# Kernel optimization log

Measured on AMD Instinct MI355X. Metric: run time of the kernel, lower is better.

The kernel has to match this reference:

```python
import jax, jax.numpy as jnp
import numpy as np

N_NODES, N_FEAT, EIG, HID = 20000, 128, 32, 64
N_EDGES = 640000
TEMP = 1.0
NUM_DROP = int(N_NODES * N_FEAT * 0.1)  # num_drop_ratio = 0.1
EPS_LOG = 1e-8


def setup_inputs() -> dict:
    key = jax.random.key(0)
    ks = jax.random.split(key, 9)
    x = jax.random.normal(ks[0], (N_NODES, N_FEAT), dtype=jnp.float32)
    edge_index = jax.random.randint(ks[1], (2, N_EDGES), 0, N_NODES, dtype=jnp.int64)
    edge_weights = jax.random.uniform(ks[2], (N_EDGES,), dtype=jnp.float32)
    x_eigen_distance = jax.random.normal(ks[3], (N_NODES, N_FEAT, EIG), dtype=jnp.float32)
    uni_rand = jax.random.uniform(ks[4], (N_NODES * N_FEAT, 2), dtype=jnp.float32,
                                  minval=1e-6, maxval=1.0 - 1e-6)
    # prob_encoder params: Linear(EIG->HID), ReLU, Linear(HID->2)
    W1 = jax.random.normal(ks[5], (EIG, HID), dtype=jnp.float32) / np.sqrt(EIG)
    b1 = jnp.zeros((HID,), dtype=jnp.float32)
    W2 = jax.random.normal(ks[6], (HID, 2), dtype=jnp.float32) / np.sqrt(HID)
    b2 = jnp.zeros((2,), dtype=jnp.float32)
    return {"x": x, "edge_index": edge_index, "edge_weights": edge_weights,
            "x_eigen_distance": x_eigen_distance, "uni_rand": uni_rand,
            "W1": W1, "b1": b1, "W2": W2, "b2": b2}


def reference(x, edge_index, edge_weights, x_eigen_distance, uni_rand, W1, b1, W2, b2):
    # flatten to [N_NODES*N_FEAT, EIG]
    flat = x_eigen_distance.reshape(-1, x_eigen_distance.shape[-1])
    h = jax.nn.relu(flat @ W1 + b1)          # [M, HID]
    logits = h @ W2 + b2                     # [M, 2]
    logits = jnp.log(jax.nn.softmax(logits, axis=1) + EPS_LOG)
    gumbel = -jnp.log(-jnp.log(uni_rand))    # gumbel noise from uniform
    y = jax.nn.softmax((logits + gumbel) / TEMP, axis=1)
    poss = jnp.clip(1.0 - y[:, 0], 1e-6, 1.0)  # [M]
    neg_vals, idx = jax.lax.top_k(-poss, NUM_DROP)  # smallest NUM_DROP
    vals = -neg_vals
    x_new = x.reshape(-1).at[idx].multiply(vals).reshape(x.shape)
    return x_new, edge_index, edge_weights
```

## Files before the change

kernel.cpp:

```cpp
#include <hip/hip_runtime.h>
#include <hip/hip_bf16.h>

#define N_NODES 20000
#define N_FEAT  128
#define EIG     32
#define HID     64
#define N_EDGES 640000
#define M_ROWS  (N_NODES * N_FEAT)
#define K_DROP  256000
#define NBINS   16384
#define LIST_CAP 4096
#define NTILES  (M_ROWS / 16)
#define NBLK    2560

#define POSS_BYTES ((size_t)M_ROWS * 4)
#define HIST_BYTES (NBINS * 4)
#define META_WORDS 16

typedef __attribute__((ext_vector_type(8))) short short8;
typedef __attribute__((ext_vector_type(4))) float floatx4;

__device__ __forceinline__ short f2bf(float f) {
  unsigned u = __float_as_uint(f);
  unsigned r = u + 0x7fffu + ((u >> 16) & 1u);
  return (short)(r >> 16);
}

__device__ __forceinline__ short2 f2bf2(float x, float y) {
  float2 f; f.x = x; f.y = y;
  __hip_bfloat162 h = __float22bfloat162_rn(f);
  union { __hip_bfloat162 h2; short2 s2; } u;
  u.h2 = h;
  return u.s2;
}

__device__ __forceinline__ int bin_of(float ps) {
  int b = (int)(ps * (float)NBINS);
  if (b > NBINS - 1) b = NBINS - 1;
  if (b < 0) b = 0;
  return b;
}

__global__ __launch_bounds__(256) void poss_kernel(
    const float* __restrict__ eig, const float* __restrict__ uni,
    const float* __restrict__ W1, const float* __restrict__ b1,
    const float* __restrict__ W2, const float* __restrict__ b2,
    float* __restrict__ poss, unsigned* __restrict__ hist)
{
  const int wave = threadIdx.x >> 6;
  const int lane = threadIdx.x & 63;
  const int col  = lane & 15;
  const int quad = lane >> 4;

  short8 bfrag[4];
  #pragma unroll
  for (int t = 0; t < 4; ++t)
    #pragma unroll
    for (int j = 0; j < 8; ++j)
      bfrag[t][j] = f2bf(W1[(quad * 8 + j) * HID + 16 * t + col]);

  float b1v[4], wd[4];
  #pragma unroll
  for (int t = 0; t < 4; ++t) {
    int n = 16 * t + col;
    b1v[t] = b1[n];
    wd[t] = W2[2 * n + 1] - W2[2 * n + 0];
  }
  const float bd = b2[1] - b2[0];

  for (int tile = blockIdx.x * 4 + wave; tile < NTILES; tile += NBLK * 4) {
    const int rowbase = tile * 16;

    const float4* pa = (const float4*)(eig + (size_t)(rowbase + col) * EIG + quad * 8);
    float4 v0 = pa[0], v1 = pa[1];
    union { short8 v; short2 h[4]; } au;
    au.h[0] = f2bf2(v0.x, v0.y);
    au.h[1] = f2bf2(v0.z, v0.w);
    au.h[2] = f2bf2(v1.x, v1.y);
    au.h[3] = f2bf2(v1.z, v1.w);

    floatx4 c[4];
    const floatx4 z = {0.f, 0.f, 0.f, 0.f};
    #pragma unroll
    for (int t = 0; t < 4; ++t)
      c[t] = __builtin_amdgcn_mfma_f32_16x16x32_bf16(au.v, bfrag[t], z, 0, 0, 0);

    float pd[4] = {0, 0, 0, 0};
    #pragma unroll
    for (int t = 0; t < 4; ++t)
      #pragma unroll
      for (int r = 0; r < 4; ++r) {
        float h = fmaxf(c[t][r] + b1v[t], 0.0f);
        pd[r] = fmaf(h, wd[t], pd[r]);
      }

    #pragma unroll
    for (int s = 1; s < 16; s <<= 1)
      #pragma unroll
      for (int r = 0; r < 4; ++r)
        pd[r] += __shfl_xor(pd[r], s, 64);

    if (col < 4) {
      int r = col;
      float ldiff = ((r == 0) ? pd[0] : (r == 1) ? pd[1] : (r == 2) ? pd[2] : pd[3]) + bd;
      int row = rowbase + quad * 4 + r;

      const float2 u = *(const float2*)(uni + (size_t)row * 2);
      float t = __expf(ldiff);
      float e1t = 1e-8f * (1.0f + t);
      float A = t + e1t;
      float B = 1.0f + e1t;
      float Lx = -__logf(u.x);
      float Ly = -__logf(u.y);
      float num = A * Lx;
      float ps = __fdividef(num, num + B * Ly);
      ps = fminf(fmaxf(ps, 1e-6f), 1.0f);
      poss[row] = ps;
      atomicAdd(&hist[bin_of(ps)], 1u);
    }
  }
}

__global__ void scan_kernel(const unsigned* __restrict__ hist, unsigned* __restrict__ meta)
{
  __shared__ unsigned psum[256];
  int t = threadIdx.x;
  unsigned s = 0;
  for (int i = 0; i < NBINS / 256; ++i) s += hist[t * (NBINS / 256) + i];
  psum[t] = s;
  __syncthreads();
  if (t == 0) {
    unsigned cum = 0;
    int c = 0;
    for (; c < 256; ++c) {
      if (cum + psum[c] >= K_DROP) break;
      cum += psum[c];
    }
    int b = c * (NBINS / 256);
    for (;; ++b) {
      unsigned h = hist[b];
      if (cum + h >= K_DROP) break;
      cum += h;
    }
    meta[0] = (unsigned)b;
    meta[1] = cum;
  }
}

__global__ __launch_bounds__(256) void collect_kernel(
    const float* __restrict__ poss, unsigned* __restrict__ meta,
    unsigned* __restrict__ list)
{
  int i = blockIdx.x * 256 + threadIdx.x;
  if (i >= M_ROWS) return;
  float ps = poss[i];
  if (bin_of(ps) == (int)meta[0]) {
    unsigned p = atomicAdd(&meta[7], 1u);
    if (p < LIST_CAP) list[p] = (unsigned)i;
  }
}

__global__ void rank_kernel(const float* __restrict__ poss,
                            const unsigned* __restrict__ list,
                            unsigned* __restrict__ meta)
{
  __shared__ unsigned sk[LIST_CAP];
  __shared__ unsigned si[LIST_CAP];
  unsigned n = meta[7];
  if (n > LIST_CAP) n = LIST_CAP;
  unsigned target = K_DROP - meta[1] - 1;
  int t = threadIdx.x;
  for (unsigned i = t; i < n; i += 256) {
    unsigned ix = list[i];
    si[i] = ix;
    sk[i] = __float_as_uint(poss[ix]);
  }
  __syncthreads();
  for (unsigned el = t; el < n; el += 256) {
    unsigned k = sk[el], ix = si[el];
    unsigned r = 0;
    for (unsigned j = 0; j < n; ++j)
      r += (sk[j] < k) || (sk[j] == k && si[j] < ix);
    if (r == target) { meta[2] = k; meta[3] = ix; }
  }
}

__global__ __launch_bounds__(256) void finalize_kernel(
    const float* __restrict__ x, const float* __restrict__ poss,
    const int* __restrict__ ei, const float* __restrict__ ew,
    const unsigned* __restrict__ meta, float* __restrict__ out)
{
  unsigned i = blockIdx.x * 256 + threadIdx.x;
  if (i < M_ROWS) {
    unsigned T = meta[2], cut = meta[3];
    float ps = poss[i];
    unsigned k = __float_as_uint(ps);
    bool sel = (k < T) || (k == T && i <= cut);
    float xv = x[i];
    out[i] = sel ? xv * ps : xv;
  } else if (i < M_ROWS + 2 * N_EDGES) {
    unsigned j = i - M_ROWS;
    out[i] = (float)ei[j];
  } else if (i < M_ROWS + 2 * N_EDGES + N_EDGES) {
    unsigned j = i - (M_ROWS + 2 * N_EDGES);
    out[i] = ew[j];
  }
}

extern "C" void kernel_launch(void* const* d_in, const int* in_sizes, int n_in,
                              void* d_out, int out_size, void* d_ws, size_t ws_size,
                              hipStream_t stream)
{
  const float* x   = (const float*)d_in[0];
  const int*   ei  = (const int*)d_in[1];
  const float* ew  = (const float*)d_in[2];
  const float* eig = (const float*)d_in[3];
  const float* uni = (const float*)d_in[4];
  const float* W1  = (const float*)d_in[5];
  const float* b1  = (const float*)d_in[6];
  const float* W2  = (const float*)d_in[7];
  const float* b2  = (const float*)d_in[8];
  float* out = (float*)d_out;

  char* ws = (char*)d_ws;
  float*    poss = (float*)ws;
  unsigned* hist = (unsigned*)(ws + POSS_BYTES);
  unsigned* meta = (unsigned*)(ws + POSS_BYTES + HIST_BYTES);
  unsigned* list = (unsigned*)(ws + POSS_BYTES + HIST_BYTES + META_WORDS * 4);

  hipMemsetAsync(hist, 0, HIST_BYTES + META_WORDS * 4 + LIST_CAP * 4, stream);
  poss_kernel<<<NBLK, 256, 0, stream>>>(eig, uni, W1, b1, W2, b2, poss, hist);
  scan_kernel<<<1, 256, 0, stream>>>(hist, meta);
  collect_kernel<<<M_ROWS / 256, 256, 0, stream>>>(poss, meta, list);
  rank_kernel<<<1, 256, 0, stream>>>(poss, list, meta);
  finalize_kernel<<<(M_ROWS + 2 * N_EDGES + N_EDGES) / 256, 256, 0, stream>>>(
      x, poss, ei, ew, meta, out);
}
```

Before: 539.1 us.

## Prefetch next tile in poss kernel, parallel scan, vectorize collect/finalize, move edge copy

The poss kernel now software-pipelines its loads, fetching the next tile's eigen rows and uniform noise while computing the current one. The single-thread histogram walk in the scan kernel is replaced by a shared-memory parallel prefix sum plus a short serial walk within one chunk. The collect and finalize kernels are vectorized to float4. The edge index/weight copy moves from finalize into collect, making finalize smaller. The prefetch raises register pressure, and these are several independent changes.

New measurement: 532.0 us. About the same (-1.3%).

```diff
diff --git a/kernel.cpp b/kernel.cpp
--- a/kernel.cpp
+++ b/kernel.cpp
@@ -51,6 +51,7 @@
   const int lane = threadIdx.x & 63;
   const int col  = lane & 15;
   const int quad = lane >> 4;
+  const int STR  = NBLK * 4;
 
   short8 bfrag[4];
   #pragma unroll
@@ -68,11 +69,29 @@
   }
   const float bd = b2[1] - b2[0];
 
-  for (int tile = blockIdx.x * 4 + wave; tile < NTILES; tile += NBLK * 4) {
+  const bool epi = (col < 4);
+  const int  epirow = quad * 4 + col;
+
+  int tile = blockIdx.x * 4 + wave;
+  float4 v0 = {0,0,0,0}, v1 = {0,0,0,0};
+  float2 u0 = {0.5f, 0.5f};
+  if (tile < NTILES) {
+    const float4* pa = (const float4*)(eig + (size_t)(tile * 16 + col) * EIG + quad * 8);
+    v0 = pa[0]; v1 = pa[1];
+    if (epi) u0 = *(const float2*)(uni + (size_t)(tile * 16 + epirow) * 2);
+  }
+
+  for (; tile < NTILES; tile += STR) {
+    const int nxt = tile + STR;
+    float4 n0 = {0,0,0,0}, n1 = {0,0,0,0};
+    float2 nu = {0.5f, 0.5f};
+    if (nxt < NTILES) {
+      const float4* pn = (const float4*)(eig + (size_t)(nxt * 16 + col) * EIG + quad * 8);
+      n0 = pn[0]; n1 = pn[1];
+      if (epi) nu = *(const float2*)(uni + (size_t)(nxt * 16 + epirow) * 2);
+    }
+
     const int rowbase = tile * 16;
-
-    const float4* pa = (const float4*)(eig + (size_t)(rowbase + col) * EIG + quad * 8);
-    float4 v0 = pa[0], v1 = pa[1];
     union { short8 v; short2 h[4]; } au;
     au.h[0] = f2bf2(v0.x, v0.y);
     au.h[1] = f2bf2(v0.z, v0.w);
@@ -100,63 +119,91 @@
       for (int r = 0; r < 4; ++r)
         pd[r] += __shfl_xor(pd[r], s, 64);
 
-    if (col < 4) {
+    if (epi) {
       int r = col;
       float ldiff = ((r == 0) ? pd[0] : (r == 1) ? pd[1] : (r == 2) ? pd[2] : pd[3]) + bd;
-      int row = rowbase + quad * 4 + r;
-
-      const float2 u = *(const float2*)(uni + (size_t)row * 2);
+      int row = rowbase + epirow;
+
       float t = __expf(ldiff);
       float e1t = 1e-8f * (1.0f + t);
       float A = t + e1t;
       float B = 1.0f + e1t;
-      float Lx = -__logf(u.x);
-      float Ly = -__logf(u.y);
+      float Lx = -__logf(u0.x);
+      float Ly = -__logf(u0.y);
       float num = A * Lx;
       float ps = __fdividef(num, num + B * Ly);
       ps = fminf(fmaxf(ps, 1e-6f), 1.0f);
       poss[row] = ps;
       atomicAdd(&hist[bin_of(ps)], 1u);
     }
+
+    v0 = n0; v1 = n1; u0 = nu;
   }
 }
 
 __global__ void scan_kernel(const unsigned* __restrict__ hist, unsigned* __restrict__ meta)
 {
   __shared__ unsigned psum[256];
+  __shared__ unsigned chunkbins[64];
+  __shared__ unsigned selc, selcum;
   int t = threadIdx.x;
   unsigned s = 0;
+  #pragma unroll 4
   for (int i = 0; i < NBINS / 256; ++i) s += hist[t * (NBINS / 256) + i];
   psum[t] = s;
   __syncthreads();
+  for (int off = 1; off < 256; off <<= 1) {
+    unsigned add = (t >= off) ? psum[t - off] : 0u;
+    __syncthreads();
+    psum[t] += add;
+    __syncthreads();
+  }
+  unsigned incl = psum[t];
+  unsigned excl = incl - s;
+  if (excl < K_DROP && K_DROP <= incl) { selc = (unsigned)t; selcum = excl; }
+  __syncthreads();
+  unsigned c = selc;
+  if (t < NBINS / 256) chunkbins[t] = hist[c * (NBINS / 256) + t];
+  __syncthreads();
   if (t == 0) {
-    unsigned cum = 0;
-    int c = 0;
-    for (; c < 256; ++c) {
-      if (cum + psum[c] >= K_DROP) break;
-      cum += psum[c];
-    }
-    int b = c * (NBINS / 256);
-    for (;; ++b) {
-      unsigned h = hist[b];
-      if (cum + h >= K_DROP) break;
+    unsigned cum = selcum;
+    int b = (int)c * (NBINS / 256);
+    for (int i = 0; i < NBINS / 256; ++i) {
+      unsigned h = chunkbins[i];
+      if (cum + h >= K_DROP) { meta[0] = (unsigned)(b + i); meta[1] = cum; break; }
       cum += h;
     }
-    meta[0] = (unsigned)b;
-    meta[1] = cum;
   }
 }
 
 __global__ __launch_bounds__(256) void collect_kernel(
     const float* __restrict__ poss, unsigned* __restrict__ meta,
-    unsigned* __restrict__ list)
+    unsigned* __restrict__ list,
+    const int* __restrict__ ei, const float* __restrict__ ew,
+    float* __restrict__ out)
 {
   int i = blockIdx.x * 256 + threadIdx.x;
-  if (i >= M_ROWS) return;
-  float ps = poss[i];
-  if (bin_of(ps) == (int)meta[0]) {
-    unsigned p = atomicAdd(&meta[7], 1u);
-    if (p < LIST_CAP) list[p] = (unsigned)i;
+  if (i < M_ROWS / 4) {
+    float4 p = ((const float4*)poss)[i];
+    int B = (int)meta[0];
+    float pp[4] = {p.x, p.y, p.z, p.w};
+    #pragma unroll
+    for (int j = 0; j < 4; ++j) {
+      if (bin_of(pp[j]) == B) {
+        unsigned q = atomicAdd(&meta[7], 1u);
+        if (q < LIST_CAP) list[q] = (unsigned)(4 * i + j);
+      }
+    }
+  } else {
+    int j = (i - M_ROWS / 4) * 4;
+    if (j < 2 * N_EDGES) {
+      int4 e = *(const int4*)(ei + j);
+      *(float4*)(out + M_ROWS + j) =
+          make_float4((float)e.x, (float)e.y, (float)e.z, (float)e.w);
+    } else {
+      int k = j - 2 * N_EDGES;
+      *(float4*)(out + M_ROWS + j) = *(const float4*)(ew + k);
+    }
   }
 }
 
@@ -187,24 +234,24 @@
 
 __global__ __launch_bounds__(256) void finalize_kernel(
     const float* __restrict__ x, const float* __restrict__ poss,
-    const int* __restrict__ ei, const float* __restrict__ ew,
     const unsigned* __restrict__ meta, float* __restrict__ out)
 {
-  unsigned i = blockIdx.x * 256 + threadIdx.x;
-  if (i < M_ROWS) {
-    unsigned T = meta[2], cut = meta[3];
-    float ps = poss[i];
-    unsigned k = __float_as_uint(ps);
-    bool sel = (k < T) || (k == T && i <= cut);
-    float xv = x[i];
-    out[i] = sel ? xv * ps : xv;
-  } else if (i < M_ROWS + 2 * N_EDGES) {
-    unsigned j = i - M_ROWS;
-    out[i] = (float)ei[j];
-  } else if (i < M_ROWS + 2 * N_EDGES + N_EDGES) {
-    unsigned j = i - (M_ROWS + 2 * N_EDGES);
-    out[i] = ew[j];
-  }
+  int i = blockIdx.x * 256 + threadIdx.x;
+  if (i >= M_ROWS / 4) return;
+  unsigned T = meta[2], cut = meta[3];
+  float4 xv = ((const float4*)x)[i];
+  float4 pv = ((const float4*)poss)[i];
+  float xx[4] = {xv.x, xv.y, xv.z, xv.w};
+  float pp[4] = {pv.x, pv.y, pv.z, pv.w};
+  float o[4];
+  #pragma unroll
+  for (int j = 0; j < 4; ++j) {
+    unsigned k = __float_as_uint(pp[j]);
+    unsigned idx = (unsigned)(4 * i + j);
+    bool sel = (k < T) || (k == T && idx <= cut);
+    o[j] = sel ? xx[j] * pp[j] : xx[j];
+  }
+  ((float4*)out)[i] = make_float4(o[0], o[1], o[2], o[3]);
 }
 
 extern "C" void kernel_launch(void* const* d_in, const int* in_sizes, int n_in,
@@ -231,8 +278,7 @@
   hipMemsetAsync(hist, 0, HIST_BYTES + META_WORDS * 4 + LIST_CAP * 4, stream);
   poss_kernel<<<NBLK, 256, 0, stream>>>(eig, uni, W1, b1, W2, b2, poss, hist);
   scan_kernel<<<1, 256, 0, stream>>>(hist, meta);
-  collect_kernel<<<M_ROWS / 256, 256, 0, stream>>>(poss, meta, list);
+  collect_kernel<<<2500 + 1875, 256, 0, stream>>>(poss, meta, list, ei, ew, out);
   rank_kernel<<<1, 256, 0, stream>>>(poss, list, meta);
-  finalize_kernel<<<(M_ROWS + 2 * N_EDGES + N_EDGES) / 256, 256, 0, stream>>>(
-      x, poss, ei, ew, meta, out);
-}
+  finalize_kernel<<<2500, 256, 0, stream>>>(x, poss, meta, out);
+}
```
